# Optimization experiments

Measured on AMD Instinct MI355X. Metric: run time of the kernel, lower is better.

The kernel has to match this reference:

```python
import jax, jax.numpy as jnp
import numpy as np

NUM_EXPERTS = 64
TOP_K = 2


def setup_inputs() -> dict:
    key = jax.random.key(0)
    k1, k2 = jax.random.split(key)
    B, D, E = 16384, 4096, NUM_EXPERTS
    routing_features = jax.random.normal(k1, (B, D), dtype=jnp.float32)
    # nn.Linear(D, E, bias=False) weight: [E, D], kaiming-uniform-ish init
    bound = 1.0 / np.sqrt(D)
    gate_w = jax.random.uniform(k2, (E, D), dtype=jnp.float32, minval=-bound, maxval=bound)
    return {"routing_features": routing_features, "gate_w": gate_w}


def reference(routing_features, gate_w):
    B = routing_features.shape[0]
    E, K = NUM_EXPERTS, TOP_K
    # linear gate (no bias): [B, E]
    logits = jnp.einsum("bd,ed->be", routing_features, gate_w)
    full_probs = jax.nn.softmax(logits, axis=-1)
    top_k_logits, top_k_indices = jax.lax.top_k(logits, K)  # [B, K]
    top_k_weights = jax.nn.softmax(top_k_logits, axis=-1)
    # load-balance loss: f_i = fraction of (token, slot) assignments to expert i
    tokens_per_expert = jnp.zeros((E,), dtype=jnp.float32).at[top_k_indices.reshape(-1)].add(1.0)
    f = tokens_per_expert / (B * K)
    P = full_probs.mean(axis=0)
    aux_loss = E * jnp.sum(f * P)
    return top_k_weights, top_k_indices, aux_loss
```

## Files before the change

### kernel.cpp

```cpp
#include <hip/hip_runtime.h>
#include <math.h>


typedef __attribute__((ext_vector_type(8))) short bf16x8;
typedef __attribute__((ext_vector_type(4))) float f32x4;

constexpr int B_ROWS  = 16384;
constexpr int D_DIM   = 4096;
constexpr int E_EXP   = 64;
constexpr int NTHR    = 512;
constexpr int GTHR    = 256;
constexpr int TM      = 64;
constexpr int KSEG    = 512;
constexpr int NSPLIT  = D_DIM / KSEG;
constexpr int NS      = KSEG / 32;
constexpr int FLAGCAP = 8192;
constexpr float GAPTHR = 1e-3f;

__device__ __forceinline__ float wave_max64(float v) {
#pragma unroll
  for (int m = 32; m >= 1; m >>= 1) v = fmaxf(v, __shfl_xor(v, m, 64));
  return v;
}
__device__ __forceinline__ float wave_sum64(float v) {
#pragma unroll
  for (int m = 32; m >= 1; m >>= 1) v += __shfl_xor(v, m, 64);
  return v;
}
__device__ __forceinline__ void wave_argmax64(float v, int i, float& mv, int& mi) {
#pragma unroll
  for (int m = 32; m >= 1; m >>= 1) {
    float ov = __shfl_xor(v, m, 64);
    int   oi = __shfl_xor(i, m, 64);
    if (ov > v || (ov == v && oi < i)) { v = ov; i = oi; }
  }
  mv = v; mi = i;
}

__device__ __forceinline__ void async_copy16(void* lds_dst, const void* g_src) {
  auto g = (const __attribute__((address_space(1))) char*)(g_src);
  auto l = (__attribute__((address_space(3))) char*)(lds_dst);
  __builtin_amdgcn_global_load_lds(g, l, 16, 0, 0);
}

__device__ __forceinline__ void split8(const f32x4 a, const f32x4 b, bf16x8& hi, bf16x8& lo) {
  float f[8] = {a[0], a[1], a[2], a[3], b[0], b[1], b[2], b[3]};
#pragma unroll
  for (int i = 0; i < 8; ++i) {
    unsigned int u = __float_as_uint(f[i]);
    hi[i] = (short)(u >> 16);
    float rem = f[i] - __uint_as_float(u & 0xffff0000u);
    lo[i] = (short)(__float_as_uint(rem) >> 16);
  }
}

__global__ __launch_bounds__(NTHR) void wsplit(const float* __restrict__ gw,
                                               char* __restrict__ wsW,
                                               unsigned int* __restrict__ hdr) {
  const int n = blockIdx.x;
  const int t = threadIdx.x;
  if (n == 0 && t < 192) hdr[t] = 0u;
  const int lane = t & 63, h = (t >> 6) & 1, wc = t >> 7;
  const int col = wc * 16 + (lane & 15);
  const int k0  = n * 32 + (lane >> 4) * 8;
  const float* src = gw + (size_t)col * D_DIM + k0;
  union { unsigned short us[8]; uint4 v; } pk;
#pragma unroll
  for (int i = 0; i < 8; ++i) {
    float f = src[i];
    unsigned int u = __float_as_uint(f);
    if (h == 0) {
      pk.us[i] = (unsigned short)(u >> 16);
    } else {
      float rem = f - __uint_as_float(u & 0xffff0000u);
      pk.us[i] = (unsigned short)(__float_as_uint(rem) >> 16);
    }
  }
  *(uint4*)(wsW + (size_t)n * 8192 + (size_t)t * 16) = pk.v;
}

__global__ __launch_bounds__(GTHR) void gemm_partial(
    const float* __restrict__ rf, const char* __restrict__ wsW,
    float* __restrict__ part) {
  __shared__ char lds[3 * 16384] __attribute__((aligned(16)));

  const int t = threadIdx.x, lane = t & 63, wv = t >> 6;
  const int rb = blockIdx.x & 255, ks = blockIdx.x >> 8;
  const int row0 = rb * TM;

  int goffA[2];
#pragma unroll
  for (int j = 0; j < 2; ++j) {
    const int q = j * GTHR + t;
    const int row = q >> 3, sl = q & 7;
    goffA[j] = (row0 + row) * D_DIM + ks * KSEG + ((sl ^ (row & 7)) << 2);
  }
  const char* wsrc = wsW + (size_t)(ks * NS) * 8192;

  const int rr  = wv * 16 + (lane & 15);
  const int s0  = (lane >> 4) * 2;
  const int a00 = rr * 128 + ((s0 ^ (rr & 7)) << 4);
  const int a01 = rr * 128 + (((s0 + 1) ^ (rr & 7)) << 4);

  f32x4 acc[4] = {{0.f,0.f,0.f,0.f},{0.f,0.f,0.f,0.f},{0.f,0.f,0.f,0.f},{0.f,0.f,0.f,0.f}};

#define ISSUE(nn)                                                            \
  {                                                                          \
    char* b_ = lds + ((nn) % 3) * 16384;                                     \
    async_copy16(b_ + t * 16, rf + goffA[0] + (nn) * 32);                    \
    async_copy16(b_ + (GTHR + t) * 16, rf + goffA[1] + (nn) * 32);           \
    async_copy16(b_ + 8192 + t * 16, wsrc + (size_t)(nn) * 8192 + t * 16);   \
    async_copy16(b_ + 8192 + (GTHR + t) * 16,                                \
                 wsrc + (size_t)(nn) * 8192 + (GTHR + t) * 16);              \
  }

  ISSUE(0);
  ISSUE(1);
#pragma unroll
  for (int n = 0; n < NS; ++n) {
    if (n + 2 < NS) {
      ISSUE(n + 2);
      asm volatile("s_waitcnt vmcnt(8)" ::: "memory");
    } else if (n + 1 < NS) {
      asm volatile("s_waitcnt vmcnt(4)" ::: "memory");
    } else {
      asm volatile("s_waitcnt vmcnt(0)" ::: "memory");
    }
    __builtin_amdgcn_s_barrier();

    const char* ab = lds + (n % 3) * 16384;
    const char* wb = ab + 8192 + lane * 16;
    const f32x4 fl = *(const f32x4*)(ab + a00);
    const f32x4 fh = *(const f32x4*)(ab + a01);
    bf16x8 ahi, alo;
    split8(fl, fh, ahi, alo);
#pragma unroll
    for (int cb = 0; cb < 4; ++cb) {
      const bf16x8 whi = *(const bf16x8*)(wb + cb * 2048);
      const bf16x8 wlo = *(const bf16x8*)(wb + cb * 2048 + 1024);
      acc[cb] = __builtin_amdgcn_mfma_f32_16x16x32_bf16(ahi, whi, acc[cb], 0, 0, 0);
      acc[cb] = __builtin_amdgcn_mfma_f32_16x16x32_bf16(alo, whi, acc[cb], 0, 0, 0);
      acc[cb] = __builtin_amdgcn_mfma_f32_16x16x32_bf16(ahi, wlo, acc[cb], 0, 0, 0);
    }
    __builtin_amdgcn_s_barrier();
  }
#undef ISSUE

  const int colb = lane & 15;
  const int rowb = (lane >> 4) * 4;
  float* dst = part + ((size_t)ks * B_ROWS + row0 + wv * 16 + rowb) * E_EXP + colb;
#pragma unroll
  for (int cb = 0; cb < 4; ++cb)
#pragma unroll
    for (int j = 0; j < 4; ++j)
      dst[(size_t)j * E_EXP + cb * 16] = acc[cb][j];
}

__global__ __launch_bounds__(NTHR) void epilogue(
    const float* __restrict__ part, float* __restrict__ out,
    float* __restrict__ psum, unsigned int* __restrict__ cnt,
    int* __restrict__ flagcnt, int* __restrict__ flaglist) {
  __shared__ float pcol[E_EXP];
  __shared__ unsigned int scnt[E_EXP];

  const int t = threadIdx.x, lane = t & 63, wv = t >> 6;
  const int row0 = blockIdx.x * 64;

  if (t < E_EXP) { scnt[t] = 0; pcol[t] = 0.f; }
  __syncthreads();

#pragma unroll
  for (int j = 0; j < 8; ++j) {
    const int row = row0 + wv * 8 + j;
    float lg = 0.f;
#pragma unroll
    for (int s = 0; s < NSPLIT; ++s)
      lg += part[((size_t)s * B_ROWS + row) * E_EXP + lane];

    const float m  = wave_max64(lg);
    const float p  = __expf(lg - m);
    const float ss = wave_sum64(p);
    atomicAdd(&pcol[lane], p / ss);

    float v1; int i1; wave_argmax64(lg, lane, v1, i1);
    const float lm1 = (lane == i1) ? -INFINITY : lg;
    float v2; int i2; wave_argmax64(lm1, lane, v2, i2);
    const float lm2 = (lane == i2) ? -INFINITY : lm1;
    float v3; int i3; wave_argmax64(lm2, lane, v3, i3);
    if (lane == 0) {
      const float ex = expf(v2 - v1);
      out[row * 2 + 0] = 1.f / (1.f + ex);
      out[row * 2 + 1] = ex / (1.f + ex);
      out[2 * B_ROWS + row * 2 + 0] = (float)i1;
      out[2 * B_ROWS + row * 2 + 1] = (float)i2;
      atomicAdd(&scnt[i1], 1u);
      atomicAdd(&scnt[i2], 1u);
      if (v1 - v2 < GAPTHR || v2 - v3 < GAPTHR) {
        int fi = atomicAdd(flagcnt, 1);
        if (fi < FLAGCAP) flaglist[fi] = row;
      }
    }
  }
  __syncthreads();
  if (t < E_EXP) {
    atomicAdd(&psum[t], pcol[t]);
    const unsigned int c = scnt[t];
    if (c) atomicAdd(&cnt[t], c);
  }
}

__global__ __launch_bounds__(256) void cleanup(
    const float* __restrict__ rf, const float* __restrict__ gw,
    const int* __restrict__ flagcnt, const int* __restrict__ flaglist,
    const float* __restrict__ psum, const unsigned int* __restrict__ cnt,
    float* __restrict__ out) {
  __shared__ double sm[256];
  const int t = threadIdx.x;
  if (blockIdx.x == 0 && t < 64) {
    const float f = (float)cnt[t] / (float)(B_ROWS * 2);
    const float P = psum[t] / (float)B_ROWS;
    float v = wave_sum64(f * P);
    if (t == 0) out[4 * B_ROWS] = (float)E_EXP * v;
  }
  const int nf = min(*flagcnt, FLAGCAP);
  for (int fi = blockIdx.x; fi < nf; fi += gridDim.x) {
    const int row = flaglist[fi];
    const int e = t & 63, seg = t >> 6;
    const float* a = rf + (size_t)row * D_DIM + seg * 1024;
    const float* w = gw + (size_t)e * D_DIM + seg * 1024;
    double p0 = 0.0, p1 = 0.0, p2 = 0.0, p3 = 0.0;
    for (int k = 0; k < 1024; k += 4) {
      p0 = fma((double)a[k + 0], (double)w[k + 0], p0);
      p1 = fma((double)a[k + 1], (double)w[k + 1], p1);
      p2 = fma((double)a[k + 2], (double)w[k + 2], p2);
      p3 = fma((double)a[k + 3], (double)w[k + 3], p3);
    }
    sm[t] = (p0 + p1) + (p2 + p3);
    __syncthreads();
    if (t < 64) {
      const double l = sm[t] + sm[64 + t] + sm[128 + t] + sm[192 + t];
      double v = l; int ii = t;
#pragma unroll
      for (int m = 32; m >= 1; m >>= 1) {
        double ov = __shfl_xor(v, m, 64); int oi = __shfl_xor(ii, m, 64);
        if (ov > v || (ov == v && oi < ii)) { v = ov; ii = oi; }
      }
      const double v1 = v; const int i1 = ii;
      const double lm = (t == i1) ? -1e300 : l;
      v = lm; ii = t;
#pragma unroll
      for (int m = 32; m >= 1; m >>= 1) {
        double ov = __shfl_xor(v, m, 64); int oi = __shfl_xor(ii, m, 64);
        if (ov > v || (ov == v && oi < ii)) { v = ov; ii = oi; }
      }
      const double v2 = v; const int i2 = ii;
      if (t == 0) {
        const double ex = exp(v2 - v1);
        out[row * 2 + 0] = (float)(1.0 / (1.0 + ex));
        out[row * 2 + 1] = (float)(ex / (1.0 + ex));
        out[2 * B_ROWS + row * 2 + 0] = (float)i1;
        out[2 * B_ROWS + row * 2 + 1] = (float)i2;
      }
    }
    __syncthreads();
  }
}

extern "C" void kernel_launch(void* const* d_in, const int* in_sizes, int n_in,
                              void* d_out, int out_size, void* d_ws, size_t ws_size,
                              hipStream_t stream) {
  const float* rf = (const float*)d_in[0];
  const float* gw = (const float*)d_in[1];
  float* out = (float*)d_out;
  float* psum = (float*)d_ws;
  unsigned int* cnt = (unsigned int*)((char*)d_ws + 256);
  int* flagcnt = (int*)((char*)d_ws + 512);
  int* flaglist = (int*)((char*)d_ws + 768);
  char* wsW = (char*)d_ws + (1u << 20);
  float* part = (float*)((char*)d_ws + (2u << 20));

  wsplit<<<D_DIM / 32, NTHR, 0, stream>>>(gw, wsW, (unsigned int*)d_ws);
  gemm_partial<<<NSPLIT * (B_ROWS / TM), GTHR, 0, stream>>>(rf, wsW, part);
  epilogue<<<B_ROWS / 64, NTHR, 0, stream>>>(part, out, psum, cnt, flagcnt, flaglist);
  cleanup<<<64, 256, 0, stream>>>(rf, gw, flagcnt, flaglist, psum, cnt, out);
}
```

Baseline: 210.4 us.

## Keep gate weights in registers and stream activation panels through LDS

The GEMM kernel is restructured so each wave holds its slice of the split bf16 gate weights in registers for the whole block, and only activation panels of 16 rows by 512 columns are streamed through double-buffered LDS. Each block now covers 256 rows across 16 panels with 512 threads, splitting the K segment between two wave groups whose partials are reduced through an LDS tile. This removes the repeated weight traffic through LDS and global memory on every K step. In exchange it adds several barriers per panel for the reduction and uses more registers, which may lower occupancy.

```diff
diff --git a/kernel.cpp b/kernel.cpp
--- a/kernel.cpp
+++ b/kernel.cpp
@@ -9,11 +9,11 @@
 constexpr int D_DIM   = 4096;
 constexpr int E_EXP   = 64;
 constexpr int NTHR    = 512;
-constexpr int GTHR    = 256;
-constexpr int TM      = 64;
+constexpr int GTHR    = 512;
 constexpr int KSEG    = 512;
 constexpr int NSPLIT  = D_DIM / KSEG;
-constexpr int NS      = KSEG / 32;
+constexpr int PROWS   = 16;
+constexpr int NPANEL  = 16;
 constexpr int FLAGCAP = 8192;
 constexpr float GAPTHR = 1e-3f;
 
@@ -82,78 +82,100 @@
 __global__ __launch_bounds__(GTHR) void gemm_partial(
     const float* __restrict__ rf, const char* __restrict__ wsW,
     float* __restrict__ part) {
-  __shared__ char lds[3 * 16384] __attribute__((aligned(16)));
+  __shared__ char apan[2][32768] __attribute__((aligned(16)));
+  __shared__ float lt[PROWS][E_EXP + 1];
 
   const int t = threadIdx.x, lane = t & 63, wv = t >> 6;
-  const int rb = blockIdx.x & 255, ks = blockIdx.x >> 8;
-  const int row0 = rb * TM;
-
-  int goffA[2];
-#pragma unroll
-  for (int j = 0; j < 2; ++j) {
+  const int cb = wv & 3, ksub = wv >> 2;
+  const int kseg = blockIdx.x & 7, rblk = blockIdx.x >> 3;
+  const int row_base = rblk * (PROWS * NPANEL);
+
+  bf16x8 wh[8], wl[8];
+  {
+    const char* wp = wsW + (size_t)(kseg * 16 + ksub * 8) * 8192
+                   + cb * 2048 + lane * 16;
+#pragma unroll
+    for (int s = 0; s < 8; ++s) {
+      wh[s] = *(const bf16x8*)(wp + (size_t)s * 8192);
+      wl[s] = *(const bf16x8*)(wp + (size_t)s * 8192 + 1024);
+    }
+  }
+  __builtin_amdgcn_sched_barrier(0);
+
+  int goffA[4];
+#pragma unroll
+  for (int j = 0; j < 4; ++j) {
     const int q = j * GTHR + t;
-    const int row = q >> 3, sl = q & 7;
-    goffA[j] = (row0 + row) * D_DIM + ks * KSEG + ((sl ^ (row & 7)) << 2);
-  }
-  const char* wsrc = wsW + (size_t)(ks * NS) * 8192;
-
-  const int rr  = wv * 16 + (lane & 15);
-  const int s0  = (lane >> 4) * 2;
-  const int a00 = rr * 128 + ((s0 ^ (rr & 7)) << 4);
-  const int a01 = rr * 128 + (((s0 + 1) ^ (rr & 7)) << 4);
-
-  f32x4 acc[4] = {{0.f,0.f,0.f,0.f},{0.f,0.f,0.f,0.f},{0.f,0.f,0.f,0.f},{0.f,0.f,0.f,0.f}};
-
-#define ISSUE(nn)                                                            \
+    const int row = q >> 7, sl = q & 127;
+    const int gs = (sl & ~7) | ((sl & 7) ^ (row & 7));
+    goffA[j] = (row_base + row) * D_DIM + kseg * KSEG + gs * 4;
+  }
+
+  const int R = lane & 15;
+
+#define ISSUE(p)                                                             \
   {                                                                          \
-    char* b_ = lds + ((nn) % 3) * 16384;                                     \
-    async_copy16(b_ + t * 16, rf + goffA[0] + (nn) * 32);                    \
-    async_copy16(b_ + (GTHR + t) * 16, rf + goffA[1] + (nn) * 32);           \
-    async_copy16(b_ + 8192 + t * 16, wsrc + (size_t)(nn) * 8192 + t * 16);   \
-    async_copy16(b_ + 8192 + (GTHR + t) * 16,                                \
-                 wsrc + (size_t)(nn) * 8192 + (GTHR + t) * 16);              \
-  }
+    char* d_ = apan[(p) & 1];                                                \
+    _Pragma("unroll") for (int j = 0; j < 4; ++j)                            \
+      async_copy16(d_ + (j * GTHR + t) * 16,                                 \
+                   rf + goffA[j] + (p) * (PROWS * D_DIM));                   \
+  }
+#define LGKM0 asm volatile("s_waitcnt lgkmcnt(0)" ::: "memory")
 
   ISSUE(0);
-  ISSUE(1);
-#pragma unroll
-  for (int n = 0; n < NS; ++n) {
-    if (n + 2 < NS) {
-      ISSUE(n + 2);
-      asm volatile("s_waitcnt vmcnt(8)" ::: "memory");
-    } else if (n + 1 < NS) {
+  for (int p = 0; p < NPANEL; ++p) {
+    if (p + 1 < NPANEL) {
+      ISSUE(p + 1);
       asm volatile("s_waitcnt vmcnt(4)" ::: "memory");
     } else {
       asm volatile("s_waitcnt vmcnt(0)" ::: "memory");
     }
     __builtin_amdgcn_s_barrier();
 
-    const char* ab = lds + (n % 3) * 16384;
-    const char* wb = ab + 8192 + lane * 16;
-    const f32x4 fl = *(const f32x4*)(ab + a00);
-    const f32x4 fh = *(const f32x4*)(ab + a01);
-    bf16x8 ahi, alo;
-    split8(fl, fh, ahi, alo);
-#pragma unroll
-    for (int cb = 0; cb < 4; ++cb) {
-      const bf16x8 whi = *(const bf16x8*)(wb + cb * 2048);
-      const bf16x8 wlo = *(const bf16x8*)(wb + cb * 2048 + 1024);
-      acc[cb] = __builtin_amdgcn_mfma_f32_16x16x32_bf16(ahi, whi, acc[cb], 0, 0, 0);
-      acc[cb] = __builtin_amdgcn_mfma_f32_16x16x32_bf16(alo, whi, acc[cb], 0, 0, 0);
-      acc[cb] = __builtin_amdgcn_mfma_f32_16x16x32_bf16(ahi, wlo, acc[cb], 0, 0, 0);
-    }
+    f32x4 acc = {0.f, 0.f, 0.f, 0.f};
+    const char* ab = apan[p & 1] + R * 2048;
+#pragma unroll
+    for (int s = 0; s < 8; ++s) {
+      const int l0 = ksub * 64 + s * 8 + (lane >> 4) * 2;
+      const int sl0 = (l0 & ~7) | ((l0 & 7) ^ (R & 7));
+      const int l1 = l0 + 1;
+      const int sl1 = (l1 & ~7) | ((l1 & 7) ^ (R & 7));
+      const f32x4 fa = *(const f32x4*)(ab + sl0 * 16);
+      const f32x4 fb = *(const f32x4*)(ab + sl1 * 16);
+      bf16x8 ahi, alo;
+      split8(fa, fb, ahi, alo);
+      acc = __builtin_amdgcn_mfma_f32_16x16x32_bf16(ahi, wh[s], acc, 0, 0, 0);
+      acc = __builtin_amdgcn_mfma_f32_16x16x32_bf16(alo, wh[s], acc, 0, 0, 0);
+      acc = __builtin_amdgcn_mfma_f32_16x16x32_bf16(ahi, wl[s], acc, 0, 0, 0);
+    }
+    LGKM0;
     __builtin_amdgcn_s_barrier();
+
+    const int colb = cb * 16 + (lane & 15);
+    const int rowb = (lane >> 4) * 4;
+    if (ksub == 0) {
+#pragma unroll
+      for (int j = 0; j < 4; ++j) lt[rowb + j][colb] = acc[j];
+    }
+    LGKM0;
+    __builtin_amdgcn_s_barrier();
+    if (ksub == 1) {
+#pragma unroll
+      for (int j = 0; j < 4; ++j) lt[rowb + j][colb] += acc[j];
+    }
+    LGKM0;
+    __builtin_amdgcn_s_barrier();
+
+    const int row0p = row_base + p * PROWS;
+#pragma unroll
+    for (int i = 0; i < 2; ++i) {
+      const int idx = i * GTHR + t;
+      const int r = idx >> 6, e = idx & 63;
+      part[((size_t)kseg * B_ROWS + row0p + r) * E_EXP + e] = lt[r][e];
+    }
   }
 #undef ISSUE
-
-  const int colb = lane & 15;
-  const int rowb = (lane >> 4) * 4;
-  float* dst = part + ((size_t)ks * B_ROWS + row0 + wv * 16 + rowb) * E_EXP + colb;
-#pragma unroll
-  for (int cb = 0; cb < 4; ++cb)
-#pragma unroll
-    for (int j = 0; j < 4; ++j)
-      dst[(size_t)j * E_EXP + cb * 16] = acc[cb][j];
+#undef LGKM0
 }
 
 __global__ __launch_bounds__(NTHR) void epilogue(
@@ -280,7 +302,7 @@
   float* part = (float*)((char*)d_ws + (2u << 20));
 
   wsplit<<<D_DIM / 32, NTHR, 0, stream>>>(gw, wsW, (unsigned int*)d_ws);
-  gemm_partial<<<NSPLIT * (B_ROWS / TM), GTHR, 0, stream>>>(rf, wsW, part);
+  gemm_partial<<<NSPLIT * (B_ROWS / (PROWS * NPANEL)), GTHR, 0, stream>>>(rf, wsW, part);
   epilogue<<<B_ROWS / 64, NTHR, 0, stream>>>(part, out, psum, cnt, flagcnt, flaglist);
   cleanup<<<64, 256, 0, stream>>>(rf, gw, flagcnt, flaglist, psum, cnt, out);
 }
```

New measurement: 223.7 us. 6.3% more time.
